# Kernel tuning notes

Measured on AMD Instinct MI355X. Metric: run time of the kernel, lower is better.

## Reference

```python
import jax, jax.numpy as jnp
import numpy as np

# Model dims (match init_kwargs)
B, H_HIST, L, C = 2, 7, 256, 512
H = H_HIST + 1          # dialogue turns after concatenating current utterance
N_HEADS = 8
N_TOP = 4               # window_size
D_HEAD = C // N_HEADS


def setup_inputs() -> dict:
    key = jax.random.key(0)
    ks = jax.random.split(key, 12)
    s = 0.02
    return {
        "global_attn_map": jax.random.normal(ks[0], (B, H, H), jnp.float32),
        "history_context": jax.random.normal(ks[1], (B, H_HIST, L, C), jnp.float32),
        "current_context": jax.random.normal(ks[2], (B, L, C), jnp.float32),
        "h_context_mask": jnp.ones((B, H_HIST, L), jnp.bool_),
        "c_context_mask": jnp.ones((B, L), jnp.bool_),
        "history_mask": jnp.ones((B, H_HIST), jnp.bool_),
        # 3 experts stacked on leading axis: 0=self, 1=past, 2=future
        "Wq": s * jax.random.normal(ks[3], (3, C, C), jnp.float32),
        "bq": jnp.zeros((3, C), jnp.float32),
        "Wk": s * jax.random.normal(ks[4], (3, C, C), jnp.float32),
        "bk": jnp.zeros((3, C), jnp.float32),
        "Wv": s * jax.random.normal(ks[5], (3, C, C), jnp.float32),
        "bv": jnp.zeros((3, C), jnp.float32),
        "Wo": s * jax.random.normal(ks[6], (3, C, C), jnp.float32),
        "bo": jnp.zeros((3, C), jnp.float32),
    }


def _mha(ctx, indx, Wq, bq, Wk, bk, Wv, bv, Wo, bo):
    """Cross-attention of every turn j (query) against its top-k gathered turns (key/value).
    ctx: (b,H,l,c), indx: (b,H,K) indices into the turn axis. Returns (b,H,K,l,c)."""
    b, Ht, l, c = ctx.shape
    K = indx.shape[-1]
    scale = 1.0 / np.sqrt(D_HEAD)
    q = (ctx @ Wq + bq).reshape(b, Ht, l, N_HEADS, D_HEAD)
    k = (ctx @ Wk + bk).reshape(b, Ht, l, N_HEADS, D_HEAD)
    v = (ctx @ Wv + bv).reshape(b, Ht, l, N_HEADS, D_HEAD)
    bidx = jnp.arange(b)[:, None, None]
    kg = k[bidx, indx]          # (b,H,K,l,nh,d)  gather KV turns
    vg = v[bidx, indx]
    scores = jnp.einsum('bhind,bhkjnd->bhknij', q, kg) * scale   # (b,H,K,nh,l,l)
    attn = jax.nn.softmax(scores, axis=-1)
    out = jnp.einsum('bhknij,bhkjnd->bhkind', attn, vg).reshape(b, Ht, K, l, c)
    return out @ Wo + bo


def _wise(ctx, attn_map, indx, Wq, bq, Wk, bk, Wv, bv, Wo, bo):
    """Vectorized form of the triple python loop: for each (batch, turn j, slot k) pick
    self/past/future expert by comparing j with indx[b,j,k], then combine weighted by attn_map."""
    outs = [_mha(ctx, indx, Wq[e], bq[e], Wk[e], bk[e], Wv[e], bv[e], Wo[e], bo[e])
            for e in range(3)]  # each (b,H,K,l,c); 0=self,1=past,2=future
    j = jnp.arange(ctx.shape[1])[None, :, None]
    sel_self = (indx == j)[..., None, None]
    sel_future = (indx > j)[..., None, None]
    combined = jnp.where(sel_self, outs[0], jnp.where(sel_future, outs[2], outs[1]))
    return jnp.einsum('bhk,bhklc->bhlc', attn_map, combined)


def reference(global_attn_map, history_context, current_context,
              h_context_mask, c_context_mask, history_mask,
              Wq, bq, Wk, bk, Wv, bv, Wo, bo):
    ctx = jnp.concatenate([history_context, current_context[:, None]], axis=1)  # (b,H,l,c)
    val, indx = jax.lax.top_k(global_attn_map, N_TOP)   # (b,H,K)
    n_attn = jax.nn.softmax(val, axis=-1)
    w = (Wq, bq, Wk, bk, Wv, bv, Wo, bo)
    h = jax.nn.relu(_wise(ctx, n_attn, indx, *w)) + ctx
    h = jax.nn.relu(_wise(h, n_attn, indx, *w)) + h
    return h
```

## Files before the change

### kernel.cpp

```cpp
#include <hip/hip_runtime.h>
#include <hip/hip_bf16.h>

constexpr int B   = 2;
constexpr int HH  = 7;
constexpr int H   = 8;
constexpr int L   = 256;
constexpr int C   = 512;
constexpr int NH  = 8;
constexpr int DH  = 64;
constexpr int KS  = 4;
constexpr int BH  = B * H;
constexpr int M4  = B * H * L;
constexpr size_t S = (size_t)B * H * L * C;

typedef __attribute__((ext_vector_type(8))) short short8;
typedef __attribute__((ext_vector_type(4))) float f32x4;
typedef unsigned short u16;
typedef unsigned int u32;

__device__ inline float bf2f(u16 u) {
    u32 x = ((u32)u) << 16;
    return __uint_as_float(x);
}
__device__ inline u16 f2bf(float f) {
    __hip_bfloat16 h = __float2bfloat16(f);
    return *reinterpret_cast<u16*>(&h);
}
__device__ inline u32 packbf(float lo, float hi) {
    return ((u32)f2bf(hi) << 16) | (u32)f2bf(lo);
}
__device__ inline void gload16(const void* g, void* l) {
    __builtin_amdgcn_global_load_lds(
        (const __attribute__((address_space(1))) void*)g,
        (__attribute__((address_space(3))) void*)l,
        16, 0, 0);
}
__device__ inline void vmcnt0() {
    asm volatile("s_waitcnt vmcnt(0)" ::: "memory");
}

__global__ __launch_bounds__(256) void concat_cast_kernel(
    const float* __restrict__ hist, const float* __restrict__ cur,
    float* __restrict__ ctx, u16* __restrict__ Xb)
{
    size_t i4 = (size_t)blockIdx.x * 256 + threadIdx.x;
    size_t elem = i4 * 4;
    int c  = (int)(elem & (C - 1));
    size_t rest = elem >> 9;
    int l  = (int)(rest & (L - 1));
    int bh = (int)(rest >> 8);
    int h  = bh & (H - 1);
    int b  = bh >> 3;
    float4 v;
    if (h < HH) {
        size_t off = ((((size_t)b * HH + h) * L + l) * C + c);
        v = *reinterpret_cast<const float4*>(hist + off);
    } else {
        size_t off = (((size_t)b * L + l) * C + c);
        v = *reinterpret_cast<const float4*>(cur + off);
    }
    *reinterpret_cast<float4*>(ctx + elem) = v;
    ushort4 o;
    o.x = f2bf(v.x); o.y = f2bf(v.y); o.z = f2bf(v.z); o.w = f2bf(v.w);
    *reinterpret_cast<ushort4*>(Xb + elem) = o;
}

__global__ void topk_kernel(const float* __restrict__ gmap,
                            float* __restrict__ attnw,
                            int* __restrict__ indxO,
                            int* __restrict__ expertO)
{
    int t = threadIdx.x;
    if (t >= BH) return;
    int h = t & (H - 1);
    const float* row = gmap + (size_t)t * H;
    float v[H];
    #pragma unroll
    for (int j = 0; j < H; ++j) v[j] = row[j];
    float sel[KS]; int si[KS];
    #pragma unroll
    for (int kk = 0; kk < KS; ++kk) {
        float best = -1e30f; int bi = 0;
        #pragma unroll
        for (int j = 0; j < H; ++j) {
            if (v[j] > best) { best = v[j]; bi = j; }
        }
        sel[kk] = best; si[kk] = bi; v[bi] = -1e30f;
    }
    float mx = sel[0];
    float w[KS]; float sum = 0.f;
    #pragma unroll
    for (int kk = 0; kk < KS; ++kk) { w[kk] = __expf(sel[kk] - mx); sum += w[kk]; }
    float inv = 1.f / sum;
    #pragma unroll
    for (int kk = 0; kk < KS; ++kk) {
        attnw[t * KS + kk] = w[kk] * inv;
        indxO[t * KS + kk] = si[kk];
        int e = (si[kk] == h) ? 0 : ((si[kk] > h) ? 2 : 1);
        expertO[t * KS + kk] = e;
    }
}

__global__ __launch_bounds__(256) void biasc_kernel(
    const float* __restrict__ bo,
    const float* __restrict__ attnw, const int* __restrict__ expertArr,
    float* __restrict__ biasC)
{
    int bh = blockIdx.x;
    float a[KS]; int e[KS];
    #pragma unroll
    for (int k = 0; k < KS; ++k) {
        a[k] = attnw[bh * KS + k];
        e[k] = expertArr[bh * KS + k];
    }
    #pragma unroll
    for (int it = 0; it < 2; ++it) {
        int c = threadIdx.x + it * 256;
        float s = 0.f;
        #pragma unroll
        for (int k = 0; k < KS; ++k)
            s += a[k] * bo[(size_t)e[k] * C + c];
        biasC[(size_t)bh * C + c] = s;
    }
}

__global__ __launch_bounds__(256) void cast_w_kernel(
    const float* __restrict__ Wq, const float* __restrict__ Wk,
    const float* __restrict__ Wv, u16* __restrict__ Wt)
{
    int p = blockIdx.z;
    int e = p / 3, t = p % 3;
    const float* W = (t == 0 ? Wq : (t == 1 ? Wk : Wv)) + (size_t)e * C * C;
    __shared__ float tile[32][33];
    int k0 = blockIdx.y * 32, n0 = blockIdx.x * 32;
    int tc = threadIdx.x & 31, tr = threadIdx.x >> 5;
    #pragma unroll
    for (int i = 0; i < 4; ++i) {
        int r = tr + i * 8;
        tile[r][tc] = W[(size_t)(k0 + r) * C + n0 + tc];
    }
    __syncthreads();
    #pragma unroll
    for (int i = 0; i < 4; ++i) {
        int r = tr + i * 8;
        Wt[(size_t)p * C * C + (size_t)(n0 + r) * C + k0 + tc] = f2bf(tile[tc][r]);
    }
}

__global__ __launch_bounds__(256) void cast_wo_kernel(
    const float* __restrict__ Wo, u16* __restrict__ Wot)
{
    int p = blockIdx.z;
    const float* W = Wo + (size_t)p * C * C;
    __shared__ float tile[32][33];
    int k0 = blockIdx.y * 32, n0 = blockIdx.x * 32;
    int tc = threadIdx.x & 31, tr = threadIdx.x >> 5;
    #pragma unroll
    for (int i = 0; i < 4; ++i) {
        int r = tr + i * 8;
        tile[r][tc] = W[(size_t)(k0 + r) * C + n0 + tc];
    }
    __syncthreads();
    #pragma unroll
    for (int i = 0; i < 4; ++i) {
        int r = tr + i * 8;
        Wot[(size_t)p * C * C + (size_t)(n0 + r) * C + k0 + tc] = f2bf(tile[tc][r]);
    }
}

__global__ __launch_bounds__(256) void proj_mfma(
    const u16* __restrict__ Xb, const u16* __restrict__ Wt,
    const float* __restrict__ bq, const float* __restrict__ bk,
    const float* __restrict__ bv,
    u16* __restrict__ out)
{
    constexpr int BK = 64;
    int p = blockIdx.z;
    int e = p / 3, t = p % 3;
    const float* bias = (t == 0 ? bq : (t == 1 ? bk : bv)) + (size_t)e * C;
    u16* Y = out + (size_t)p * S;
    const u16* Wp = Wt + (size_t)p * C * C;

    int m0 = blockIdx.y * 128;
    int n0 = blockIdx.x * 128;

    __shared__ u16 As[128 * BK];
    __shared__ u16 Bs[128 * BK];

    int tid  = threadIdx.x;
    int lane = tid & 63;
    int wid  = tid >> 6;
    int wr = wid >> 1, wc = wid & 1;

    f32x4 acc[4][4];
    #pragma unroll
    for (int m = 0; m < 4; ++m)
        #pragma unroll
        for (int n = 0; n < 4; ++n)
            acc[m][n] = (f32x4){0.f, 0.f, 0.f, 0.f};

    int rowA = wr * 64 + (lane & 15);
    int rowB = wc * 64 + (lane & 15);
    int kgrp = 8 * (lane >> 4);

    for (int kt = 0; kt < C / BK; ++kt) {
        int k0 = kt * BK;
        #pragma unroll
        for (int j = 0; j < 4; ++j) {
            int chunk = (wid * 4 + j) * 64 + lane;
            int r  = chunk >> 3;
            int cb = chunk & 7;
            int ksw = (cb ^ (r & 7)) << 3;
            gload16(Xb + (size_t)(m0 + r) * C + k0 + ksw, &As[(wid * 4 + j) * 512]);
            gload16(Wp + (size_t)(n0 + r) * C + k0 + ksw, &Bs[(wid * 4 + j) * 512]);
        }
        __syncthreads();
        const char* Ab = (const char*)As;
        const char* Bb = (const char*)Bs;
        #pragma unroll
        for (int ks = 0; ks < 2; ++ks) {
            int kb2 = (ks * 32 + kgrp) * 2;
            short8 af[4], bfr[4];
            #pragma unroll
            for (int m = 0; m < 4; ++m) {
                int row = rowA + m * 16;
                af[m] = *reinterpret_cast<const short8*>(
                    Ab + ((row * 128 + kb2) ^ ((row & 7) << 4)));
            }
            #pragma unroll
            for (int n = 0; n < 4; ++n) {
                int row = rowB + n * 16;
                bfr[n] = *reinterpret_cast<const short8*>(
                    Bb + ((row * 128 + kb2) ^ ((row & 7) << 4)));
            }
            #pragma unroll
            for (int m = 0; m < 4; ++m)
                #pragma unroll
                for (int n = 0; n < 4; ++n)
                    acc[m][n] = __builtin_amdgcn_mfma_f32_16x16x32_bf16(
                        af[m], bfr[n], acc[m][n], 0, 0, 0);
        }
        __syncthreads();
    }

    int colb = n0 + wc * 64 + (lane & 15);
    int rowb = m0 + wr * 64 + (lane >> 4) * 4;
    #pragma unroll
    for (int n = 0; n < 4; ++n) {
        int col = colb + n * 16;
        float bcol = bias[col];
        #pragma unroll
        for (int m = 0; m < 4; ++m) {
            #pragma unroll
            for (int r = 0; r < 4; ++r) {
                int row = rowb + m * 16 + r;
                Y[(size_t)row * C + col] = f2bf(acc[m][n][r] + bcol);
            }
        }
    }
}

__global__ __launch_bounds__(256) void attn_mfma(
    const u16* __restrict__ qkv,
    const int* __restrict__ indx, const int* __restrict__ expertArr,
    const float* __restrict__ attnw,
    u16* __restrict__ Obuf)
{
    int head = blockIdx.x;
    int slot = blockIdx.y;
    int z    = blockIdx.z;
    int bh   = z >> 1, qh = z & 1;
    int b    = bh >> 3;
    int mi   = bh * KS + slot;
    int src  = indx[mi];
    int e    = expertArr[mi];
    float ak = attnw[mi];
    int qbase = qh * 128;

    const u16* qp = qkv + (size_t)(e * 3 + 0) * S + (size_t)bh * L * C + head * DH;
    const u16* kp = qkv + (size_t)(e * 3 + 1) * S + (size_t)(b * H + src) * L * C + head * DH;
    const u16* vp = qkv + (size_t)(e * 3 + 2) * S + (size_t)(b * H + src) * L * C + head * DH;

    __shared__ u16 Ks[64 * 64];
    __shared__ u16 Vt[64 * 64];
    __shared__ u16 Pl[4][32 * 64];

    int tid = threadIdx.x, lane = tid & 63, w = tid >> 6;
    int c = lane & 15, gl = lane >> 4;
    int qoff = qbase + w * 32;

    short8 qf[2][2];
    #pragma unroll
    for (int n = 0; n < 2; ++n)
        #pragma unroll
        for (int kf = 0; kf < 2; ++kf)
            qf[n][kf] = *reinterpret_cast<const short8*>(
                qp + (size_t)(qoff + n * 16 + c) * C + kf * 32 + 8 * gl);

    f32x4 accO[4][2];
    #pragma unroll
    for (int m = 0; m < 4; ++m)
        #pragma unroll
        for (int n = 0; n < 2; ++n)
            accO[m][n] = (f32x4){0.f, 0.f, 0.f, 0.f};
    float mrun[2], lrun[2];
    #pragma unroll
    for (int n = 0; n < 2; ++n) { mrun[n] = -1e30f; lrun[n] = 0.f; }

    char* Plw = (char*)&Pl[w][0];

    for (int t = 0; t < 4; ++t) {
        int c0 = t * 64;
        __syncthreads();
        #pragma unroll
        for (int it = 0; it < 2; ++it) {
            int ch = tid + 256 * it;
            int r = ch >> 3, cb = ch & 7;
            short8 kv = *reinterpret_cast<const short8*>(kp + (size_t)(c0 + r) * C + cb * 8);
            int ad = (r * 128 + cb * 16) ^ ((r & 7) << 4);
            *reinterpret_cast<short8*>((char*)Ks + ad) = kv;
        }
        {
            int rp = tid & 31;
            int d0 = (tid >> 5) * 8;
            const u16* v0p = vp + (size_t)(c0 + 2 * rp) * C + d0;
            const u16* v1p = v0p + C;
            ushort4 a0 = *reinterpret_cast<const ushort4*>(v0p);
            ushort4 a1 = *reinterpret_cast<const ushort4*>(v0p + 4);
            ushort4 b0 = *reinterpret_cast<const ushort4*>(v1p);
            ushort4 b1 = *reinterpret_cast<const ushort4*>(v1p + 4);
            u16 va[8] = {a0.x, a0.y, a0.z, a0.w, a1.x, a1.y, a1.z, a1.w};
            u16 vb[8] = {b0.x, b0.y, b0.z, b0.w, b1.x, b1.y, b1.z, b1.w};
            #pragma unroll
            for (int j = 0; j < 8; ++j) {
                u32 pk = ((u32)vb[j] << 16) | (u32)va[j];
                int ad = ((d0 + j) * 128 + rp * 4) ^ (((d0 + j) & 7) << 4);
                *reinterpret_cast<u32*>((char*)Vt + ad) = pk;
            }
        }
        __syncthreads();

        f32x4 accS[4][2];
        #pragma unroll
        for (int m = 0; m < 4; ++m)
            #pragma unroll
            for (int n = 0; n < 2; ++n)
                accS[m][n] = (f32x4){0.f, 0.f, 0.f, 0.f};
        #pragma unroll
        for (int kf = 0; kf < 2; ++kf) {
            short8 ka[4];
            #pragma unroll
            for (int m = 0; m < 4; ++m) {
                int row = m * 16 + c;
                ka[m] = *reinterpret_cast<const short8*>(
                    (char*)Ks + ((row * 128 + (kf * 32 + 8 * gl) * 2) ^ ((row & 7) << 4)));
            }
            #pragma unroll
            for (int m = 0; m < 4; ++m)
                #pragma unroll
                for (int n = 0; n < 2; ++n)
                    accS[m][n] = __builtin_amdgcn_mfma_f32_16x16x32_bf16(
                        ka[m], qf[n][kf], accS[m][n], 0, 0, 0);
        }

        #pragma unroll
        for (int n = 0; n < 2; ++n) {
            float tm = -1e30f;
            #pragma unroll
            for (int m = 0; m < 4; ++m)
                #pragma unroll
                for (int r = 0; r < 4; ++r)
                    tm = fmaxf(tm, accS[m][n][r] * 0.125f);
            tm = fmaxf(tm, __shfl_xor(tm, 16));
            tm = fmaxf(tm, __shfl_xor(tm, 32));
            float nm = fmaxf(mrun[n], tm);
            float al = __expf(mrun[n] - nm);
            mrun[n] = nm;
            lrun[n] *= al;
            #pragma unroll
            for (int m = 0; m < 4; ++m)
                #pragma unroll
                for (int r = 0; r < 4; ++r)
                    accO[m][n][r] *= al;
            float ps = 0.f;
            #pragma unroll
            for (int m = 0; m < 4; ++m)
                #pragma unroll
                for (int r = 0; r < 4; ++r) {
                    float pv = __expf(accS[m][n][r] * 0.125f - nm);
                    accS[m][n][r] = pv;
                    ps += pv;
                }
            lrun[n] += ps;
            int row = n * 16 + c;
            int sw = (row & 7) << 4;
            #pragma unroll
            for (int m = 0; m < 4; ++m) {
                u32 p0 = packbf(accS[m][n][0], accS[m][n][1]);
                u32 p1 = packbf(accS[m][n][2], accS[m][n][3]);
                int base = row * 128 + (m * 16 + 4 * gl) * 2;
                *reinterpret_cast<u32*>(Plw + (base ^ sw)) = p0;
                *reinterpret_cast<u32*>(Plw + ((base + 4) ^ sw)) = p1;
            }
        }

        #pragma unroll
        for (int kf = 0; kf < 2; ++kf) {
            short8 va[4], pb[2];
            #pragma unroll
            for (int m = 0; m < 4; ++m) {
                int row = m * 16 + c;
                va[m] = *reinterpret_cast<const short8*>(
                    (char*)Vt + ((row * 128 + (kf * 32 + 8 * gl) * 2) ^ ((row & 7) << 4)));
            }
            #pragma unroll
            for (int n = 0; n < 2; ++n) {
                int row = n * 16 + c;
                pb[n] = *reinterpret_cast<const short8*>(
                    Plw + ((row * 128 + (kf * 32 + 8 * gl) * 2) ^ ((row & 7) << 4)));
            }
            #pragma unroll
            for (int m = 0; m < 4; ++m)
                #pragma unroll
                for (int n = 0; n < 2; ++n)
                    accO[m][n] = __builtin_amdgcn_mfma_f32_16x16x32_bf16(
                        va[m], pb[n], accO[m][n], 0, 0, 0);
        }
    }

    float inv[2];
    #pragma unroll
    for (int n = 0; n < 2; ++n) {
        float lv = lrun[n];
        lv += __shfl_xor(lv, 16);
        lv += __shfl_xor(lv, 32);
        inv[n] = ak / lv;
    }
    #pragma unroll
    for (int m = 0; m < 4; ++m)
        #pragma unroll
        for (int n = 0; n < 2; ++n) {
            int row = n * 16 + c;
            int sw = (row & 7) << 4;
            float o0 = accO[m][n][0] * inv[n];
            float o1 = accO[m][n][1] * inv[n];
            float o2 = accO[m][n][2] * inv[n];
            float o3 = accO[m][n][3] * inv[n];
            int base = row * 128 + (m * 16 + 4 * gl) * 2;
            *reinterpret_cast<u32*>(Plw + (base ^ sw)) = packbf(o0, o1);
            *reinterpret_cast<u32*>(Plw + ((base + 4) ^ sw)) = packbf(o2, o3);
        }
    #pragma unroll
    for (int it = 0; it < 4; ++it) {
        int q = it * 8 + (lane >> 3), cb = lane & 7;
        short8 ov = *reinterpret_cast<const short8*>(
            Plw + ((q * 128 + cb * 16) ^ ((q & 7) << 4)));
        *reinterpret_cast<short8*>(
            Obuf + ((size_t)mi * L + qoff + q) * C + head * DH + cb * 8) = ov;
    }
}

__global__ __launch_bounds__(256) void wo_fused_mfma(
    const u16* __restrict__ Obuf, const u16* __restrict__ Wot,
    const int* __restrict__ expertArr,
    float* __restrict__ wise)
{
    constexpr int BK = 64;
    int bh = blockIdx.z;
    int m0 = blockIdx.y * 64;
    int n0 = blockIdx.x * 128;

    int e4[KS];
    #pragma unroll
    for (int k = 0; k < KS; ++k) e4[k] = expertArr[bh * KS + k];

    __shared__ u16 As[2][64 * BK];
    __shared__ u16 Bs[2][128 * BK];

    int tid = threadIdx.x, lane = tid & 63, wid = tid >> 6;
    int wr = wid >> 1, wc = wid & 1;
    int c = lane & 15, gl = lane >> 4;

    f32x4 acc[2][4];
    #pragma unroll
    for (int m = 0; m < 2; ++m)
        #pragma unroll
        for (int n = 0; n < 4; ++n)
            acc[m][n] = (f32x4){0.f, 0.f, 0.f, 0.f};

    auto stage = [&](int bb, int kt) {
        int slot = kt >> 3;
        int k0   = (kt & 7) * BK;
        const u16* Ap = Obuf + ((size_t)(bh * KS + slot) * L + m0) * C + k0;
        const u16* Bp = Wot + (size_t)e4[slot] * C * C + (size_t)n0 * C + k0;
        #pragma unroll
        for (int it = 0; it < 2; ++it) {
            int base = wid * 64 + it * 256;
            int ch = base + lane;
            int r = ch >> 3, cb = ch & 7;
            int ksw = (cb ^ (r & 7)) << 3;
            gload16(Ap + (size_t)r * C + ksw, &As[bb][base * 8]);
        }
        #pragma unroll
        for (int j = 0; j < 4; ++j) {
            int base = (wid * 4 + j) * 64;
            int ch = base + lane;
            int r = ch >> 3, cb = ch & 7;
            int ksw = (cb ^ (r & 7)) << 3;
            gload16(Bp + (size_t)r * C + ksw, &Bs[bb][base * 8]);
        }
    };

    stage(0, 0);
    vmcnt0();
    __syncthreads();

    constexpr int NT = 4 * (C / BK);
    for (int kt = 0; kt < NT; ++kt) {
        int bb = kt & 1;
        if (kt + 1 < NT) stage(bb ^ 1, kt + 1);
        const char* Ab = (const char*)&As[bb][0];
        const char* Bb = (const char*)&Bs[bb][0];
        #pragma unroll
        for (int ks = 0; ks < 2; ++ks) {
            int kb2 = (ks * 32 + 8 * gl) * 2;
            short8 af[2], bfr[4];
            #pragma unroll
            for (int m = 0; m < 2; ++m) {
                int row = wr * 32 + m * 16 + c;
                af[m] = *reinterpret_cast<const short8*>(
                    Ab + ((row * 128 + kb2) ^ ((row & 7) << 4)));
            }
            #pragma unroll
            for (int n = 0; n < 4; ++n) {
                int row = wc * 64 + n * 16 + c;
                bfr[n] = *reinterpret_cast<const short8*>(
                    Bb + ((row * 128 + kb2) ^ ((row & 7) << 4)));
            }
            #pragma unroll
            for (int m = 0; m < 2; ++m)
                #pragma unroll
                for (int n = 0; n < 4; ++n)
                    acc[m][n] = __builtin_amdgcn_mfma_f32_16x16x32_bf16(
                        af[m], bfr[n], acc[m][n], 0, 0, 0);
        }
        if (kt + 1 < NT) {
            vmcnt0();
            __syncthreads();
        }
    }

    float* wbh = wise + (size_t)bh * L * C;
    #pragma unroll
    for (int m = 0; m < 2; ++m) {
        #pragma unroll
        for (int r = 0; r < 4; ++r) {
            int row = m0 + wr * 32 + m * 16 + 4 * gl + r;
            #pragma unroll
            for (int n = 0; n < 4; ++n) {
                int col = n0 + wc * 64 + n * 16 + c;
                wbh[(size_t)row * C + col] = acc[m][n][r];
            }
        }
    }
}

__global__ __launch_bounds__(256) void ew_relu_add_cast(
    const float* __restrict__ wise, const float* __restrict__ biasC,
    const float* __restrict__ xin,
    float* __restrict__ xout, u16* __restrict__ Xb)
{
    size_t i4 = (size_t)blockIdx.x * 256 + threadIdx.x;
    size_t elem = i4 * 4;
    int cc = (int)(elem & (C - 1));
    int bh = (int)(elem >> 17);
    float4 w = *reinterpret_cast<const float4*>(wise + elem);
    float4 bsv = *reinterpret_cast<const float4*>(biasC + (size_t)bh * C + cc);
    float4 x = *reinterpret_cast<const float4*>(xin + elem);
    float4 o;
    o.x = fmaxf(w.x + bsv.x, 0.f) + x.x;
    o.y = fmaxf(w.y + bsv.y, 0.f) + x.y;
    o.z = fmaxf(w.z + bsv.z, 0.f) + x.z;
    o.w = fmaxf(w.w + bsv.w, 0.f) + x.w;
    *reinterpret_cast<float4*>(xout + elem) = o;
    ushort4 ob;
    ob.x = f2bf(o.x); ob.y = f2bf(o.y); ob.z = f2bf(o.z); ob.w = f2bf(o.w);
    *reinterpret_cast<ushort4*>(Xb + elem) = ob;
}

extern "C" void kernel_launch(void* const* d_in, const int* in_sizes, int n_in,
                              void* d_out, int out_size, void* d_ws, size_t ws_size,
                              hipStream_t stream) {
    const float* gmap = (const float*)d_in[0];
    const float* hist = (const float*)d_in[1];
    const float* cur  = (const float*)d_in[2];
    const float* Wq   = (const float*)d_in[6];
    const float* bq   = (const float*)d_in[7];
    const float* Wk   = (const float*)d_in[8];
    const float* bk   = (const float*)d_in[9];
    const float* Wv   = (const float*)d_in[10];
    const float* bv   = (const float*)d_in[11];
    const float* Wo   = (const float*)d_in[12];
    const float* bo   = (const float*)d_in[13];
    float* outp       = (float*)d_out;

    char* ws = (char*)d_ws;
    float* ctx  = (float*)(ws);
    float* x1   = (float*)(ws + 4 * S);
    float* wise = (float*)(ws + 8 * S);
    u16*   qkv  = (u16*)(ws + 12 * S);
    u16*   Obuf = (u16*)(ws + 30 * S);
    char*  tail = ws + 38 * S;
    float* attnw  = (float*)(tail);
    int*   indx   = (int*)(tail + 256);
    int*   expert = (int*)(tail + 512);
    float* biasC  = (float*)(tail + 1024);
    u16*   Wot    = (u16*)(tail + 64 * 1024);
    u16*   Xb     = (u16*)(tail + 2 * 1024 * 1024);
    u16*   Wt     = (u16*)(tail + 8 * 1024 * 1024);

    dim3 projGrid(C / 128, M4 / 128, 9);
    dim3 castWGrid(C / 32, C / 32, 9);
    dim3 castWoGrid(C / 32, C / 32, 3);
    dim3 attnGrid(NH, KS, BH * 2);
    dim3 woGrid(C / 128, L / 64, BH);
    int ewBlocks = (int)(S / 4 / 256);

    concat_cast_kernel<<<ewBlocks, 256, 0, stream>>>(hist, cur, ctx, Xb);
    topk_kernel<<<1, 64, 0, stream>>>(gmap, attnw, indx, expert);
    biasc_kernel<<<BH, 256, 0, stream>>>(bo, attnw, expert, biasC);
    cast_wo_kernel<<<castWoGrid, 256, 0, stream>>>(Wo, Wot);
    cast_w_kernel<<<castWGrid, 256, 0, stream>>>(Wq, Wk, Wv, Wt);

    proj_mfma<<<projGrid, 256, 0, stream>>>(Xb, Wt, bq, bk, bv, qkv);
    attn_mfma<<<attnGrid, 256, 0, stream>>>(qkv, indx, expert, attnw, Obuf);
    wo_fused_mfma<<<woGrid, 256, 0, stream>>>(Obuf, Wot, expert, wise);
    ew_relu_add_cast<<<ewBlocks, 256, 0, stream>>>(wise, biasC, ctx, x1, Xb);

    proj_mfma<<<projGrid, 256, 0, stream>>>(Xb, Wt, bq, bk, bv, qkv);
    attn_mfma<<<attnGrid, 256, 0, stream>>>(qkv, indx, expert, attnw, Obuf);
    wo_fused_mfma<<<woGrid, 256, 0, stream>>>(Obuf, Wot, expert, wise);
    ew_relu_add_cast<<<ewBlocks, 256, 0, stream>>>(wise, biasC, x1, outp, Xb);
}
```

Baseline: 203.7 us.

## Double-buffer QKV projection GEMM and fuse relu-residual epilogue into Wo kernel

The QKV projection kernel moves from a single-buffered BK=64 loop to a double-buffered BK=32 loop with a new swizzle, so the next tile's global loads can overlap MFMA work on the current one. Separately, the bias-add, ReLU, residual add and bf16 cast formerly done by a standalone elementwise kernel now run in the Wo GEMM epilogue. This removes the fp32 'wise' intermediate round-trip and two kernel launches. The fused epilogue uses scalar, less coalesced stores, and the smaller K-tile means more barriers per GEMM.

```diff
diff --git a/kernel.cpp b/kernel.cpp
--- a/kernel.cpp
+++ b/kernel.cpp
@@ -174,7 +174,8 @@
     const float* __restrict__ bv,
     u16* __restrict__ out)
 {
-    constexpr int BK = 64;
+    constexpr int BK = 32;
+    constexpr int NT = C / BK;
     int p = blockIdx.z;
     int e = p / 3, t = p % 3;
     const float* bias = (t == 0 ? bq : (t == 1 ? bk : bv)) + (size_t)e * C;
@@ -184,13 +185,14 @@
     int m0 = blockIdx.y * 128;
     int n0 = blockIdx.x * 128;
 
-    __shared__ u16 As[128 * BK];
-    __shared__ u16 Bs[128 * BK];
+    __shared__ u16 As[2][128 * BK];
+    __shared__ u16 Bs[2][128 * BK];
 
     int tid  = threadIdx.x;
     int lane = tid & 63;
     int wid  = tid >> 6;
     int wr = wid >> 1, wc = wid & 1;
+    int c = lane & 15, gl = lane >> 4;
 
     f32x4 acc[4][4];
     #pragma unroll
@@ -199,52 +201,69 @@
         for (int n = 0; n < 4; ++n)
             acc[m][n] = (f32x4){0.f, 0.f, 0.f, 0.f};
 
-    int rowA = wr * 64 + (lane & 15);
-    int rowB = wc * 64 + (lane & 15);
-    int kgrp = 8 * (lane >> 4);
-
-    for (int kt = 0; kt < C / BK; ++kt) {
+    int rowA = wr * 64 + c;
+    int rowB = wc * 64 + c;
+
+    auto stage = [&](int bb, int kt) {
         int k0 = kt * BK;
         #pragma unroll
-        for (int j = 0; j < 4; ++j) {
-            int chunk = (wid * 4 + j) * 64 + lane;
-            int r  = chunk >> 3;
-            int cb = chunk & 7;
-            int ksw = (cb ^ (r & 7)) << 3;
-            gload16(Xb + (size_t)(m0 + r) * C + k0 + ksw, &As[(wid * 4 + j) * 512]);
-            gload16(Wp + (size_t)(n0 + r) * C + k0 + ksw, &Bs[(wid * 4 + j) * 512]);
-        }
-        __syncthreads();
-        const char* Ab = (const char*)As;
-        const char* Bb = (const char*)Bs;
-        #pragma unroll
-        for (int ks = 0; ks < 2; ++ks) {
-            int kb2 = (ks * 32 + kgrp) * 2;
-            short8 af[4], bfr[4];
-            #pragma unroll
-            for (int m = 0; m < 4; ++m) {
-                int row = rowA + m * 16;
-                af[m] = *reinterpret_cast<const short8*>(
-                    Ab + ((row * 128 + kb2) ^ ((row & 7) << 4)));
-            }
-            #pragma unroll
-            for (int n = 0; n < 4; ++n) {
-                int row = rowB + n * 16;
-                bfr[n] = *reinterpret_cast<const short8*>(
-                    Bb + ((row * 128 + kb2) ^ ((row & 7) << 4)));
-            }
-            #pragma unroll
-            for (int m = 0; m < 4; ++m)
-                #pragma unroll
-                for (int n = 0; n < 4; ++n)
-                    acc[m][n] = __builtin_amdgcn_mfma_f32_16x16x32_bf16(
-                        af[m], bfr[n], acc[m][n], 0, 0, 0);
-        }
-        __syncthreads();
-    }
-
-    int colb = n0 + wc * 64 + (lane & 15);
-    int rowb = m0 + wr * 64 + (lane >> 4) * 4;
+        for (int it = 0; it < 2; ++it) {
+            int base = it * 256 + wid * 64;
+            int ch = base + lane;
+            int r = ch >> 2, s = ch & 3;
+            int r_src = r ^ ((r >> 2) & 1);
+            int s_src = s ^ (r_src & 3);
+            gload16(Xb + (size_t)(m0 + r_src) * C + k0 + s_src * 8,
+                    &As[bb][base * 8]);
+        }
+        #pragma unroll
+        for (int it = 0; it < 2; ++it) {
+            int base = it * 256 + wid * 64;
+            int ch = base + lane;
+            int r = ch >> 2, s = ch & 3;
+            int r_src = r ^ ((r >> 2) & 1);
+            int s_src = s ^ (r_src & 3);
+            gload16(Wp + (size_t)(n0 + r_src) * C + k0 + s_src * 8,
+                    &Bs[bb][base * 8]);
+        }
+    };
+
+    stage(0, 0);
+    vmcnt0();
+    __syncthreads();
+
+    for (int kt = 0; kt < NT; ++kt) {
+        int bb = kt & 1;
+        if (kt + 1 < NT) stage(bb ^ 1, kt + 1);
+        const char* Ab = (const char*)&As[bb][0];
+        const char* Bb = (const char*)&Bs[bb][0];
+        short8 af[4], bfr[4];
+        #pragma unroll
+        for (int m = 0; m < 4; ++m) {
+            int row = rowA + m * 16;
+            af[m] = *reinterpret_cast<const short8*>(
+                Ab + ((row * 64 + gl * 16) ^ ((row & 7) << 4)));
+        }
+        #pragma unroll
+        for (int n = 0; n < 4; ++n) {
+            int row = rowB + n * 16;
+            bfr[n] = *reinterpret_cast<const short8*>(
+                Bb + ((row * 64 + gl * 16) ^ ((row & 7) << 4)));
+        }
+        #pragma unroll
+        for (int m = 0; m < 4; ++m)
+            #pragma unroll
+            for (int n = 0; n < 4; ++n)
+                acc[m][n] = __builtin_amdgcn_mfma_f32_16x16x32_bf16(
+                    af[m], bfr[n], acc[m][n], 0, 0, 0);
+        if (kt + 1 < NT) {
+            vmcnt0();
+            __syncthreads();
+        }
+    }
+
+    int colb = n0 + wc * 64 + c;
+    int rowb = m0 + wr * 64 + gl * 4;
     #pragma unroll
     for (int n = 0; n < 4; ++n) {
         int col = colb + n * 16;
@@ -460,10 +479,11 @@
     }
 }
 
-__global__ __launch_bounds__(256) void wo_fused_mfma(
+__global__ __launch_bounds__(256) void wo_fused_ew(
     const u16* __restrict__ Obuf, const u16* __restrict__ Wot,
-    const int* __restrict__ expertArr,
-    float* __restrict__ wise)
+    const int* __restrict__ expertArr, const float* __restrict__ biasC,
+    const float* __restrict__ xin,
+    float* __restrict__ xout, u16* __restrict__ XbOut)
 {
     constexpr int BK = 64;
     int bh = blockIdx.z;
@@ -550,7 +570,13 @@
         }
     }
 
-    float* wbh = wise + (size_t)bh * L * C;
+    const float* xr = xin + (size_t)bh * L * C;
+    float* xo = xout + (size_t)bh * L * C;
+    u16*   xb = XbOut + (size_t)bh * L * C;
+    float biasS[4];
+    #pragma unroll
+    for (int n = 0; n < 4; ++n)
+        biasS[n] = biasC[(size_t)bh * C + n0 + wc * 64 + n * 16 + c];
     #pragma unroll
     for (int m = 0; m < 2; ++m) {
         #pragma unroll
@@ -559,33 +585,13 @@
             #pragma unroll
             for (int n = 0; n < 4; ++n) {
                 int col = n0 + wc * 64 + n * 16 + c;
-                wbh[(size_t)row * C + col] = acc[m][n][r];
-            }
-        }
-    }
-}
-
-__global__ __launch_bounds__(256) void ew_relu_add_cast(
-    const float* __restrict__ wise, const float* __restrict__ biasC,
-    const float* __restrict__ xin,
-    float* __restrict__ xout, u16* __restrict__ Xb)
-{
-    size_t i4 = (size_t)blockIdx.x * 256 + threadIdx.x;
-    size_t elem = i4 * 4;
-    int cc = (int)(elem & (C - 1));
-    int bh = (int)(elem >> 17);
-    float4 w = *reinterpret_cast<const float4*>(wise + elem);
-    float4 bsv = *reinterpret_cast<const float4*>(biasC + (size_t)bh * C + cc);
-    float4 x = *reinterpret_cast<const float4*>(xin + elem);
-    float4 o;
-    o.x = fmaxf(w.x + bsv.x, 0.f) + x.x;
-    o.y = fmaxf(w.y + bsv.y, 0.f) + x.y;
-    o.z = fmaxf(w.z + bsv.z, 0.f) + x.z;
-    o.w = fmaxf(w.w + bsv.w, 0.f) + x.w;
-    *reinterpret_cast<float4*>(xout + elem) = o;
-    ushort4 ob;
-    ob.x = f2bf(o.x); ob.y = f2bf(o.y); ob.z = f2bf(o.z); ob.w = f2bf(o.w);
-    *reinterpret_cast<ushort4*>(Xb + elem) = ob;
+                float v = acc[m][n][r] + biasS[n];
+                float o = fmaxf(v, 0.f) + xr[(size_t)row * C + col];
+                xo[(size_t)row * C + col] = o;
+                xb[(size_t)row * C + col] = f2bf(o);
+            }
+        }
+    }
 }
 
 extern "C" void kernel_launch(void* const* d_in, const int* in_sizes, int n_in,
@@ -607,7 +613,6 @@
     char* ws = (char*)d_ws;
     float* ctx  = (float*)(ws);
     float* x1   = (float*)(ws + 4 * S);
-    float* wise = (float*)(ws + 8 * S);
     u16*   qkv  = (u16*)(ws + 12 * S);
     u16*   Obuf = (u16*)(ws + 30 * S);
     char*  tail = ws + 38 * S;
@@ -634,11 +639,9 @@
 
     proj_mfma<<<projGrid, 256, 0, stream>>>(Xb, Wt, bq, bk, bv, qkv);
     attn_mfma<<<attnGrid, 256, 0, stream>>>(qkv, indx, expert, attnw, Obuf);
-    wo_fused_mfma<<<woGrid, 256, 0, stream>>>(Obuf, Wot, expert, wise);
-    ew_relu_add_cast<<<ewBlocks, 256, 0, stream>>>(wise, biasC, ctx, x1, Xb);
+    wo_fused_ew<<<woGrid, 256, 0, stream>>>(Obuf, Wot, expert, biasC, ctx, x1, Xb);
 
     proj_mfma<<<projGrid, 256, 0, stream>>>(Xb, Wt, bq, bk, bv, qkv);
     attn_mfma<<<attnGrid, 256, 0, stream>>>(qkv, indx, expert, attnw, Obuf);
-    wo_fused_mfma<<<woGrid, 256, 0, stream>>>(Obuf, Wot, expert, wise);
-    ew_relu_add_cast<<<ewBlocks, 256, 0, stream>>>(wise, biasC, x1, outp, Xb);
-}
+    wo_fused_ew<<<woGrid, 256, 0, stream>>>(Obuf, Wot, expert, biasC, x1, outp, Xb);
+}
```

Measured after the change: 187.4 us. 1.09x faster.
